# Optimization experiments

Measured on AMD Instinct MI355X. Metric: run time of the kernel, lower is better.

The kernel has to match this reference:

```python
import jax, jax.numpy as jnp
import numpy as np

B, T, D = 4, 2048, 512
H, P = 8, 16
DH = D // H
C = 512
HF = WF = 64
RADIUS = 0.08


def setup_inputs() -> dict:
    key = jax.random.key(0)
    ks = jax.random.split(key, 8)
    s = 0.02
    return {
        "q": jax.random.normal(ks[0], (B, T, D), jnp.float32),
        "fmap": jax.random.normal(ks[1], (B, C, HF, WF), jnp.float32),
        "ref_xy": jax.random.uniform(ks[2], (B, T, 2), jnp.float32),
        # params ((in,out) layout; equals torch Linear with W.T)
        "Wv": jax.random.normal(ks[3], (C, D), jnp.float32) * s,      # 1x1 conv, no bias
        "W_off": jax.random.normal(ks[4], (D, H * P * 2), jnp.float32) * s,
        "b_off": jnp.zeros((H * P * 2,), jnp.float32),
        "W_w": jax.random.normal(ks[5], (D, H * P), jnp.float32) * s,
        "b_w": jnp.zeros((H * P,), jnp.float32),
        "W_out": jax.random.normal(ks[6], (D, D), jnp.float32) * s,
        "b_out": jnp.zeros((D,), jnp.float32),
    }


def _deform_attn(q, fmap, ref_xy, Wv, W_off, b_off, W_w, b_w, W_out, b_out):
    Bq, Tq, Dm = q.shape
    _, Cc, Hf, Wf = fmap.shape
    dh = Dm // H
    # value projection (1x1 conv) then split heads: (B,H,dh,Hf,Wf)
    v = jnp.einsum("bchw,cd->bdhw", fmap, Wv).reshape(Bq, H, dh, Hf, Wf)
    # flatten spatial for gather: (B,H,Hf*Wf,dh)
    vflat = v.transpose(0, 1, 3, 4, 2).reshape(Bq, H, Hf * Wf, dh)

    off = (q @ W_off + b_off).reshape(Bq, Tq, H, P, 2)
    attn = jax.nn.softmax((q @ W_w + b_w).reshape(Bq, Tq, H, P), axis=-1)

    samp = ref_xy[:, :, None, None, :] + RADIUS * off   # (B,T,H,P,2) in ~[0,1]
    g = samp * 2.0 - 1.0                                 # grid coords in [-1,1]
    # align_corners=True mapping to pixel coords
    ix = (g[..., 0] + 1.0) * 0.5 * (Wf - 1)              # (B,T,H,P)
    iy = (g[..., 1] + 1.0) * 0.5 * (Hf - 1)
    ix0 = jnp.floor(ix)
    iy0 = jnp.floor(iy)
    fx = ix - ix0
    fy = iy - iy0
    ix0i = ix0.astype(jnp.int32)
    iy0i = iy0.astype(jnp.int32)

    def corner(xi, yi, wgt):
        # wgt: bilinear weight * attention weight, (B,T,H,P)
        valid = (xi >= 0) & (xi < Wf) & (yi >= 0) & (yi < Hf)  # zeros padding
        xi_c = jnp.clip(xi, 0, Wf - 1)
        yi_c = jnp.clip(yi, 0, Hf - 1)
        idx = (yi_c * Wf + xi_c).transpose(0, 2, 1, 3).reshape(Bq, H, Tq * P)
        gat = jnp.take_along_axis(vflat, idx[..., None], axis=2)  # (B,H,T*P,dh)
        wm = (wgt * valid).transpose(0, 2, 1, 3).reshape(Bq, H, Tq * P)
        return gat * wm[..., None]

    # fold softmax weights into bilinear corner weights, then sum over points
    feat = (
        corner(ix0i,     iy0i,     (1 - fx) * (1 - fy) * attn)
        + corner(ix0i + 1, iy0i,     fx * (1 - fy) * attn)
        + corner(ix0i,     iy0i + 1, (1 - fx) * fy * attn)
        + corner(ix0i + 1, iy0i + 1, fx * fy * attn)
    )  # (B,H,T*P,dh)
    ctx = feat.reshape(Bq, H, Tq, P, dh).sum(axis=3)     # (B,H,T,dh)
    ctx = ctx.transpose(0, 2, 1, 3).reshape(Bq, Tq, Dm)  # concat heads
    return ctx @ W_out + b_out


def reference(q, fmap, ref_xy, Wv, W_off, b_off, W_w, b_w, W_out, b_out):
    return _deform_attn(q, fmap, ref_xy, Wv, W_off, b_off, W_w, b_w, W_out, b_out)
```

## Files before the change

### kernel.cpp

```cpp
#include <hip/hip_runtime.h>
#include <hip/hip_bf16.h>
#include <math.h>

constexpr int Bsz = 4, T = 2048, Hh = 8;
constexpr int HFi = 64, WFi = 64;
constexpr float RADIUS = 0.08f;

typedef __bf16 bf16x8 __attribute__((ext_vector_type(8)));
typedef float f32x4 __attribute__((ext_vector_type(4)));
typedef unsigned short u16x8 __attribute__((ext_vector_type(8)));

typedef const __attribute__((address_space(1))) void* gcptr;
typedef __attribute__((address_space(3))) void* lptr;

#define GLOAD_LDS16(g, l) \
  __builtin_amdgcn_global_load_lds((gcptr)(const void*)(g), (lptr)(void*)(l), 16, 0, 0)

union BU { __hip_bfloat16 b; unsigned short u; };

__global__ __launch_bounds__(256) void prep_kernel(
    const float* __restrict__ q, __hip_bfloat16* __restrict__ qsplit,
    const float* __restrict__ W_off, const float* __restrict__ W_w,
    const float* __restrict__ b_off, const float* __restrict__ b_w,
    __hip_bfloat16* __restrict__ Wcat, float* __restrict__ bias_cat,
    const float* __restrict__ Wv, __hip_bfloat16* __restrict__ WvT,
    const float* __restrict__ W_out, __hip_bfloat16* __restrict__ WoutT,
    const float* __restrict__ fmap, __hip_bfloat16* __restrict__ fmapT) {
  __shared__ float tile[64][65];
  const int blk = blockIdx.x;
  const int tid = threadIdx.x;
  if (blk < 4096) {
    const int idx = blk * 256 + tid;
    const int m = idx >> 7, kq = (idx & 127) * 4;
    float4 v = *(const float4*)&q[(size_t)m * 512 + kq];
    union { __hip_bfloat16 b[4]; ushort4 u; } hi, lo;
    float f[4] = {v.x, v.y, v.z, v.w};
#pragma unroll
    for (int i = 0; i < 4; ++i) {
      hi.b[i] = __float2bfloat16(f[i]);
      lo.b[i] = __float2bfloat16(f[i] - __bfloat162float(hi.b[i]));
    }
    *(ushort4*)&qsplit[(size_t)m * 1024 + kq] = hi.u;
    *(ushort4*)&qsplit[(size_t)m * 1024 + 512 + kq] = lo.u;
    return;
  }
  if (blk < 6400) {
    const int idx = (blk - 4096) * 256 + tid;
    const int n = idx / 1536, kp = idx % 1536;
    const int k = kp & 511;
    const float w = (n < 256) ? W_off[(size_t)k * 256 + n]
                              : W_w[(size_t)k * 128 + (n - 256)];
    const __hip_bfloat16 h = __float2bfloat16(w);
    const __hip_bfloat16 o =
        (kp < 1024) ? h : __float2bfloat16(w - __bfloat162float(h));
    Wcat[(size_t)n * 1536 + kp] = o;
    if (idx < 384) bias_cat[idx] = (idx < 256) ? b_off[idx] : b_w[idx - 256];
    return;
  }
  const float* src;
  __hip_bfloat16* dst;
  int ldin, ldout, r0, c0;
  if (blk < 6528) {
    const int t2 = blk - 6400;
    src = (t2 < 64) ? Wv : W_out;
    dst = (t2 < 64) ? WvT : WoutT;
    ldin = 512; ldout = 512;
    const int tl = t2 & 63;
    r0 = (tl >> 3) * 64; c0 = (tl & 7) * 64;
  } else {
    const int t3 = blk - 6528;
    const int b = t3 >> 9;
    const int tl = t3 & 511;
    r0 = (tl >> 6) * 64;
    c0 = (tl & 63) * 64;
    src = fmap + (size_t)b * 512 * 4096;
    dst = fmapT + (size_t)b * 4096 * 512;
    ldin = 4096; ldout = 512;
  }
  {
    const int tr = tid >> 2;
    const int tc = (tid & 3) * 16;
    const float* s = &src[(size_t)(r0 + tr) * ldin + c0 + tc];
#pragma unroll
    for (int j4 = 0; j4 < 4; ++j4) {
      float4 v = *(const float4*)&s[j4 * 4];
      tile[tr][tc + j4 * 4 + 0] = v.x;
      tile[tr][tc + j4 * 4 + 1] = v.y;
      tile[tr][tc + j4 * 4 + 2] = v.z;
      tile[tr][tc + j4 * 4 + 3] = v.w;
    }
    __syncthreads();
    const int oc = tid >> 2;
    const int rb = (tid & 3) * 16;
    u16x8 o0, o1;
#pragma unroll
    for (int j = 0; j < 8; ++j) {
      BU a, bz;
      a.b = __float2bfloat16(tile[rb + j][oc]);
      bz.b = __float2bfloat16(tile[rb + 8 + j][oc]);
      o0[j] = a.u;
      o1[j] = bz.u;
    }
    __hip_bfloat16* d = &dst[(size_t)(c0 + oc) * ldout + r0 + rb];
    *(u16x8*)d = o0;
    *(u16x8*)(d + 8) = o1;
  }
}

__global__ __launch_bounds__(256) void fused_gemm(
    const __hip_bfloat16* __restrict__ qsplit,
    const __hip_bfloat16* __restrict__ Wcat,
    const float* __restrict__ bias_cat, float* __restrict__ projbuf,
    const __hip_bfloat16* __restrict__ fmapT,
    const __hip_bfloat16* __restrict__ WvT, __hip_bfloat16* __restrict__ vflat) {
  __shared__ unsigned short lds[2 * 128 * 64];
  unsigned short* As = lds;
  unsigned short* Bs = lds + 128 * 64;
  const int blk = blockIdx.x;
  const int tid = threadIdx.x;
  const int lane = tid & 63;
  const int wave = tid >> 6;
  const int l15 = lane & 15, quad = lane >> 4;
  const int srow = lane >> 3;
  const int scol = (((lane & 7) ^ srow) * 8);
  const int fxor = (l15 & 7) * 8;

  if (blk < 384) {
    const int m0 = (blk & 63) * 128;
    const int n0 = (blk >> 6) * 64;
    const int wm = (wave & 1) * 64, wn = (wave >> 1) * 32;
    f32x4 acc[4][2] = {};
    for (int k0 = 0; k0 < 1536; k0 += 64) {
      const int ka = (k0 >= 1024) ? k0 - 1024 : k0;
#pragma unroll
      for (int i = 0; i < 4; ++i) {
        const int j = wave * 4 + i;
        const int r = j * 8 + srow;
        GLOAD_LDS16(qsplit + (size_t)(m0 + r) * 1024 + ka + scol, As + j * 512);
      }
#pragma unroll
      for (int i = 0; i < 2; ++i) {
        const int j = wave * 2 + i;
        const int r = j * 8 + srow;
        GLOAD_LDS16(Wcat + (size_t)(n0 + r) * 1536 + k0 + scol, Bs + j * 512);
      }
      __syncthreads();
#pragma unroll
      for (int ks = 0; ks < 2; ++ks) {
        bf16x8 af[4], bfr[2];
#pragma unroll
        for (int i = 0; i < 4; ++i)
          af[i] = *(const bf16x8*)&As[(wm + i * 16 + l15) * 64 + ((ks * 32 + quad * 8) ^ fxor)];
#pragma unroll
        for (int j = 0; j < 2; ++j)
          bfr[j] = *(const bf16x8*)&Bs[(wn + j * 16 + l15) * 64 + ((ks * 32 + quad * 8) ^ fxor)];
#pragma unroll
        for (int i = 0; i < 4; ++i)
#pragma unroll
          for (int j = 0; j < 2; ++j)
            acc[i][j] = __builtin_amdgcn_mfma_f32_16x16x32_bf16(af[i], bfr[j], acc[i][j], 0, 0, 0);
      }
      __syncthreads();
    }
#pragma unroll
    for (int i = 0; i < 4; ++i) {
      const int mbase = m0 + wm + i * 16 + quad * 4;
#pragma unroll
      for (int j = 0; j < 2; ++j) {
        const int n = n0 + wn + j * 16 + l15;
        const float bb = bias_cat[n];
#pragma unroll
        for (int r = 0; r < 4; ++r)
          projbuf[(size_t)(mbase + r) * 384 + n] = acc[i][j][r] + bb;
      }
    }
  } else {
    const int vb = blk - 384;
    const int b = vb >> 7, rr = vb & 127;
    const int m0 = (rr >> 2) * 128;
    const int n0 = (rr & 3) * 128;
    const __hip_bfloat16* A = fmapT + (size_t)b * 4096 * 512;
    __hip_bfloat16* vout = vflat + (size_t)b * 8 * 4096 * 64;
    const int wm = (wave & 1) * 64, wn = (wave >> 1) * 64;
    f32x4 acc[4][4] = {};
    for (int k0 = 0; k0 < 512; k0 += 64) {
#pragma unroll
      for (int i = 0; i < 4; ++i) {
        const int j = wave * 4 + i;
        const int r = j * 8 + srow;
        GLOAD_LDS16(A + (size_t)(m0 + r) * 512 + k0 + scol, As + j * 512);
        GLOAD_LDS16(WvT + (size_t)(n0 + r) * 512 + k0 + scol, Bs + j * 512);
      }
      __syncthreads();
#pragma unroll
      for (int ks = 0; ks < 2; ++ks) {
        bf16x8 af[4], bfr[4];
#pragma unroll
        for (int i = 0; i < 4; ++i)
          af[i] = *(const bf16x8*)&As[(wm + i * 16 + l15) * 64 + ((ks * 32 + quad * 8) ^ fxor)];
#pragma unroll
        for (int j = 0; j < 4; ++j)
          bfr[j] = *(const bf16x8*)&Bs[(wn + j * 16 + l15) * 64 + ((ks * 32 + quad * 8) ^ fxor)];
#pragma unroll
        for (int i = 0; i < 4; ++i)
#pragma unroll
          for (int j = 0; j < 4; ++j)
            acc[i][j] = __builtin_amdgcn_mfma_f32_16x16x32_bf16(af[i], bfr[j], acc[i][j], 0, 0, 0);
      }
      __syncthreads();
    }
    unsigned short* Ct = lds;
#pragma unroll
    for (int i = 0; i < 4; ++i) {
#pragma unroll
      for (int j = 0; j < 4; ++j) {
        const int ngl = wn + j * 16 + l15;
#pragma unroll
        for (int r = 0; r < 4; ++r) {
          const int sl = wm + i * 16 + quad * 4 + r;
          BU u;
          u.b = __float2bfloat16(acc[i][j][r]);
          Ct[sl * 128 + (ngl ^ (((sl >> 2) & 3) * 16))] = u.u;
        }
      }
    }
    __syncthreads();
#pragma unroll
    for (int c = 0; c < 8; ++c) {
      const int sl = (tid >> 4) + c * 16;
      const int chunk = tid & 15;
      const int head = (n0 >> 6) + (chunk >> 3);
      const int dh = (chunk & 7) * 8;
      const int e = (chunk * 8) ^ (((sl >> 2) & 3) * 16);
      *(u16x8*)(vout + (size_t)head * (4096 * 64) + (size_t)(m0 + sl) * 64 + dh) =
          *(const u16x8*)&Ct[sl * 128 + e];
    }
  }
}

__global__ __launch_bounds__(256) void sample_kernel(
    const float* __restrict__ ref_xy, const float* __restrict__ projbuf,
    const unsigned int* __restrict__ vflat2, unsigned int* __restrict__ ctx2) {
  __shared__ float4 wsm[8][16];
  __shared__ int bsm[8][16];
  const int blk = blockIdx.x;
  const int bt = (blk & 7) * 1024 + (blk >> 3);
  const int b = bt >> 11;
  const int tid = threadIdx.x;
  const int wave = tid >> 6;
  const int lane = tid & 63;
  const int l31 = lane & 31;
  const bool hiHalf = lane >= 32;

  if (tid < 64) {
    const int h = tid >> 3, pi = tid & 7;
    const float ref_x = ref_xy[bt * 2 + 0];
    const float ref_y = ref_xy[bt * 2 + 1];
    const float* prow = projbuf + (size_t)bt * 384;
    const float* lg = prow + 256 + h * 16;
    float lv[16];
    float mx = -1e30f;
#pragma unroll
    for (int p = 0; p < 16; ++p) {
      lv[p] = lg[p];
      mx = fmaxf(mx, lv[p]);
    }
    float sum = 0.f;
#pragma unroll
    for (int p = 0; p < 16; ++p) {
      lv[p] = __expf(lv[p] - mx);
      sum += lv[p];
    }
    const float inv = 1.0f / sum;
    const float* of = prow + h * 32;
#pragma unroll
    for (int pq = 0; pq < 2; ++pq) {
      const int p = pi + pq * 8;
      const float aw = inv * lv[p];
      const float2 o2 = *(const float2*)&of[p * 2];
      const float ix = (ref_x + RADIUS * o2.x) * (float)(WFi - 1);
      const float iy = (ref_y + RADIUS * o2.y) * (float)(HFi - 1);
      const float ix0f = floorf(ix), iy0f = floorf(iy);
      const float fx = ix - ix0f, fy = iy - iy0f;
      const int ix0 = (int)ix0f, iy0 = (int)iy0f;

      float wx0 = 1.f - fx, wx1 = fx;
      float wy0 = 1.f - fy, wy1 = fy;
      if (ix0 == -1) { wx0 = fx; wx1 = 0.f; }
      if (ix0 == 63) { wx0 = 0.f; wx1 = 1.f - fx; }
      if (ix0 < -1 || ix0 > 63) { wx0 = 0.f; wx1 = 0.f; }
      if (iy0 == -1) { wy0 = fy; wy1 = 0.f; }
      if (iy0 == 63) { wy0 = 0.f; wy1 = 1.f - fy; }
      if (iy0 < -1 || iy0 > 63) { wy0 = 0.f; wy1 = 0.f; }
      const int xA = min(max(ix0, 0), WFi - 2);
      const int yA = min(max(iy0, 0), HFi - 2);

      wsm[h][p] = make_float4(wx0, wx1, wy0 * aw, wy1 * aw);
      bsm[h][p] = (yA * WFi + xA) * 32;
    }
  }
  __syncthreads();

  for (int h = wave; h < Hh; h += 4) {
    const float4* wq = &wsm[h][hiHalf ? 8 : 0];
    const int* bq = &bsm[h][hiHalf ? 8 : 0];
    const unsigned int* vb = vflat2 + (size_t)(b * 8 + h) * (4096 * 32) + l31;

    float acc0 = 0.f, acc1 = 0.f;
#pragma unroll
    for (int pp = 0; pp < 8; ++pp) {
      const float4 w4 = wq[pp];
      const unsigned int* r0 = vb + bq[pp];

      const unsigned int v00 = r0[0], v10 = r0[32];
      const unsigned int v01 = r0[2048], v11 = r0[2080];

      const float w00 = w4.x * w4.z, w10 = w4.y * w4.z;
      const float w01 = w4.x * w4.w, w11 = w4.y * w4.w;

      const float e00 = __uint_as_float(v00 << 16), o00 = __uint_as_float(v00 & 0xffff0000u);
      const float e10 = __uint_as_float(v10 << 16), o10 = __uint_as_float(v10 & 0xffff0000u);
      const float e01 = __uint_as_float(v01 << 16), o01 = __uint_as_float(v01 & 0xffff0000u);
      const float e11 = __uint_as_float(v11 << 16), o11 = __uint_as_float(v11 & 0xffff0000u);

      acc0 = fmaf(w00, e00, acc0);
      acc1 = fmaf(w00, o00, acc1);
      acc0 = fmaf(w10, e10, acc0);
      acc1 = fmaf(w10, o10, acc1);
      acc0 = fmaf(w01, e01, acc0);
      acc1 = fmaf(w01, o01, acc1);
      acc0 = fmaf(w11, e11, acc0);
      acc1 = fmaf(w11, o11, acc1);
    }

    acc0 += __shfl_xor(acc0, 32, 64);
    acc1 += __shfl_xor(acc1, 32, 64);
    if (!hiHalf) {
      BU c0, c1;
      c0.b = __float2bfloat16(acc0);
      c1.b = __float2bfloat16(acc1);
      ctx2[(size_t)bt * 256 + h * 32 + l31] = ((unsigned int)c1.u << 16) | c0.u;
    }
  }
}

__global__ __launch_bounds__(256) void outproj_kernel(
    const __hip_bfloat16* __restrict__ A, const __hip_bfloat16* __restrict__ Bm,
    const float* __restrict__ bias, float* __restrict__ C) {
  __shared__ unsigned short As[128 * 64];
  __shared__ unsigned short Bs[128 * 64];
  const int tid = threadIdx.x;
  const int lane = tid & 63;
  const int wave = tid >> 6;
  const int wm = (wave & 1) * 64, wn = (wave >> 1) * 64;
  const int l15 = lane & 15, quad = lane >> 4;
  const int m0 = blockIdx.x * 128, n0 = blockIdx.y * 128;
  const int srow = lane >> 3;
  const int scol = (((lane & 7) ^ srow) * 8);
  const int fxor = (l15 & 7) * 8;

  f32x4 acc[4][4] = {};

  for (int k0 = 0; k0 < 512; k0 += 64) {
#pragma unroll
    for (int i = 0; i < 4; ++i) {
      const int j = wave * 4 + i;
      const int r = j * 8 + srow;
      GLOAD_LDS16(A + (size_t)(m0 + r) * 512 + k0 + scol, As + j * 512);
      GLOAD_LDS16(Bm + (size_t)(n0 + r) * 512 + k0 + scol, Bs + j * 512);
    }
    __syncthreads();
#pragma unroll
    for (int ks = 0; ks < 2; ++ks) {
      bf16x8 af[4], bfr[4];
#pragma unroll
      for (int i = 0; i < 4; ++i)
        af[i] = *(const bf16x8*)&As[(wm + i * 16 + l15) * 64 + ((ks * 32 + quad * 8) ^ fxor)];
#pragma unroll
      for (int j = 0; j < 4; ++j)
        bfr[j] = *(const bf16x8*)&Bs[(wn + j * 16 + l15) * 64 + ((ks * 32 + quad * 8) ^ fxor)];
#pragma unroll
      for (int i = 0; i < 4; ++i)
#pragma unroll
        for (int j = 0; j < 4; ++j)
          acc[i][j] = __builtin_amdgcn_mfma_f32_16x16x32_bf16(af[i], bfr[j], acc[i][j], 0, 0, 0);
    }
    __syncthreads();
  }

#pragma unroll
  for (int i = 0; i < 4; ++i) {
    const int mbase = m0 + wm + i * 16 + quad * 4;
#pragma unroll
    for (int j = 0; j < 4; ++j) {
      const int n = n0 + wn + j * 16 + l15;
      const float bb = bias[n];
#pragma unroll
      for (int r = 0; r < 4; ++r)
        C[(size_t)(mbase + r) * 512 + n] = acc[i][j][r] + bb;
    }
  }
}

extern "C" void kernel_launch(void* const* d_in, const int* in_sizes, int n_in,
                              void* d_out, int out_size, void* d_ws, size_t ws_size,
                              hipStream_t stream) {
  const float* q      = (const float*)d_in[0];
  const float* fmap   = (const float*)d_in[1];
  const float* ref_xy = (const float*)d_in[2];
  const float* Wv     = (const float*)d_in[3];
  const float* W_off  = (const float*)d_in[4];
  const float* b_off  = (const float*)d_in[5];
  const float* W_w    = (const float*)d_in[6];
  const float* b_w    = (const float*)d_in[7];
  const float* W_out  = (const float*)d_in[8];
  const float* b_out  = (const float*)d_in[9];
  float* out = (float*)d_out;

  char* ws = (char*)d_ws;
  __hip_bfloat16* qsplit = (__hip_bfloat16*)ws; ws += (size_t)8192 * 1024 * 2;
  __hip_bfloat16* Wcat   = (__hip_bfloat16*)ws; ws += (size_t)384 * 1536 * 2;
  float* bias_cat        = (float*)ws;          ws += 384 * 4;
  float* projbuf         = (float*)ws;          ws += (size_t)8192 * 384 * 4;
  __hip_bfloat16* fmapT  = (__hip_bfloat16*)ws; ws += (size_t)4 * 4096 * 512 * 2;
  __hip_bfloat16* WvT    = (__hip_bfloat16*)ws; ws += (size_t)512 * 512 * 2;
  __hip_bfloat16* WoutT  = (__hip_bfloat16*)ws; ws += (size_t)512 * 512 * 2;
  __hip_bfloat16* vflat  = (__hip_bfloat16*)ws; ws += (size_t)4 * 8 * 4096 * 64 * 2;
  __hip_bfloat16* ctxb   = (__hip_bfloat16*)ws; ws += (size_t)8192 * 512 * 2;

  prep_kernel<<<dim3(8576), 256, 0, stream>>>(
      q, qsplit, W_off, W_w, b_off, b_w, Wcat, bias_cat, Wv, WvT, W_out, WoutT,
      fmap, fmapT);

  fused_gemm<<<dim3(896), 256, 0, stream>>>(
      qsplit, Wcat, bias_cat, projbuf, fmapT, WvT, vflat);

  sample_kernel<<<dim3(Bsz * T), 256, 0, stream>>>(
      ref_xy, projbuf, (const unsigned int*)vflat, (unsigned int*)ctxb);

  outproj_kernel<<<dim3(64, 4), 256, 0, stream>>>(ctxb, WoutT, b_out, out);
}
```

Measured before the change: 187.4 us.

## Restructure sampling kernel to one query per wave with 8-byte gathers

The sampling kernel now handles four queries per block, one per wave, instead of one query per block with a single 64-thread wave doing setup. The softmax over points is computed cooperatively with lane shuffles rather than serially per thread. Gathers use 8-byte uint2 loads (4 bf16 channels per lane), with 16 lanes covering a head row and four lane groups splitting the points, reduced by shuffles. This aims to use all threads in setup, cut block count and launch overhead, and widen memory accesses, at the cost of more shuffle reductions and more registers per lane.

New measurement: 192.0 us. 2.5% more time.

```diff
diff --git a/kernel.cpp b/kernel.cpp
--- a/kernel.cpp
+++ b/kernel.cpp
@@ -17,6 +17,13 @@
   __builtin_amdgcn_global_load_lds((gcptr)(const void*)(g), (lptr)(void*)(l), 16, 0, 0)
 
 union BU { __hip_bfloat16 b; unsigned short u; };
+
+__device__ __forceinline__ float bflo(unsigned int u) {
+  return __uint_as_float(u << 16);
+}
+__device__ __forceinline__ float bfhi(unsigned int u) {
+  return __uint_as_float(u & 0xffff0000u);
+}
 
 __global__ __launch_bounds__(256) void prep_kernel(
     const float* __restrict__ q, __hip_bfloat16* __restrict__ qsplit,
@@ -240,43 +247,38 @@
 
 __global__ __launch_bounds__(256) void sample_kernel(
     const float* __restrict__ ref_xy, const float* __restrict__ projbuf,
-    const unsigned int* __restrict__ vflat2, unsigned int* __restrict__ ctx2) {
-  __shared__ float4 wsm[8][16];
-  __shared__ int bsm[8][16];
+    const uint2* __restrict__ vflat2, uint2* __restrict__ ctx2) {
+  __shared__ float4 wsm[4][8][16];
+  __shared__ int bsm[4][8][16];
   const int blk = blockIdx.x;
-  const int bt = (blk & 7) * 1024 + (blk >> 3);
-  const int b = bt >> 11;
   const int tid = threadIdx.x;
   const int wave = tid >> 6;
   const int lane = tid & 63;
-  const int l31 = lane & 31;
-  const bool hiHalf = lane >= 32;
-
-  if (tid < 64) {
-    const int h = tid >> 3, pi = tid & 7;
+  const int bt = (blk & 7) * 1024 + (blk >> 3) * 4 + wave;
+  const int b = bt >> 11;
+
+  {
+    const int h = lane >> 3, pi = lane & 7;
     const float ref_x = ref_xy[bt * 2 + 0];
     const float ref_y = ref_xy[bt * 2 + 1];
     const float* prow = projbuf + (size_t)bt * 384;
     const float* lg = prow + 256 + h * 16;
-    float lv[16];
-    float mx = -1e30f;
-#pragma unroll
-    for (int p = 0; p < 16; ++p) {
-      lv[p] = lg[p];
-      mx = fmaxf(mx, lv[p]);
-    }
-    float sum = 0.f;
-#pragma unroll
-    for (int p = 0; p < 16; ++p) {
-      lv[p] = __expf(lv[p] - mx);
-      sum += lv[p];
-    }
-    const float inv = 1.0f / sum;
+    const float l0 = lg[pi], l1 = lg[pi + 8];
+    float mx = fmaxf(l0, l1);
+    mx = fmaxf(mx, __shfl_xor(mx, 1, 64));
+    mx = fmaxf(mx, __shfl_xor(mx, 2, 64));
+    mx = fmaxf(mx, __shfl_xor(mx, 4, 64));
+    const float e0 = __expf(l0 - mx), e1 = __expf(l1 - mx);
+    float s = e0 + e1;
+    s += __shfl_xor(s, 1, 64);
+    s += __shfl_xor(s, 2, 64);
+    s += __shfl_xor(s, 4, 64);
+    const float inv = 1.0f / s;
     const float* of = prow + h * 32;
 #pragma unroll
-    for (int pq = 0; pq < 2; ++pq) {
-      const int p = pi + pq * 8;
-      const float aw = inv * lv[p];
+    for (int q = 0; q < 2; ++q) {
+      const int p = pi + q * 8;
+      const float aw = inv * (q ? e1 : e0);
       const float2 o2 = *(const float2*)&of[p * 2];
       const float ix = (ref_x + RADIUS * o2.x) * (float)(WFi - 1);
       const float iy = (ref_y + RADIUS * o2.y) * (float)(HFi - 1);
@@ -295,51 +297,62 @@
       const int xA = min(max(ix0, 0), WFi - 2);
       const int yA = min(max(iy0, 0), HFi - 2);
 
-      wsm[h][p] = make_float4(wx0, wx1, wy0 * aw, wy1 * aw);
-      bsm[h][p] = (yA * WFi + xA) * 32;
+      wsm[wave][h][p] = make_float4(wx0, wx1, wy0 * aw, wy1 * aw);
+      bsm[wave][h][p] = (yA * WFi + xA) * 16;
     }
   }
   __syncthreads();
 
-  for (int h = wave; h < Hh; h += 4) {
-    const float4* wq = &wsm[h][hiHalf ? 8 : 0];
-    const int* bq = &bsm[h][hiHalf ? 8 : 0];
-    const unsigned int* vb = vflat2 + (size_t)(b * 8 + h) * (4096 * 32) + l31;
-
-    float acc0 = 0.f, acc1 = 0.f;
-#pragma unroll
-    for (int pp = 0; pp < 8; ++pp) {
-      const float4 w4 = wq[pp];
-      const unsigned int* r0 = vb + bq[pp];
-
-      const unsigned int v00 = r0[0], v10 = r0[32];
-      const unsigned int v01 = r0[2048], v11 = r0[2080];
-
+  const int g = lane >> 4, sub = lane & 15;
+#pragma unroll
+  for (int h = 0; h < Hh; ++h) {
+    const uint2* vb = vflat2 + (size_t)(b * 8 + h) * (4096 * 16) + sub;
+    float a0 = 0.f, a1 = 0.f, a2 = 0.f, a3 = 0.f;
+#pragma unroll
+    for (int it = 0; it < 4; ++it) {
+      const int p = g * 4 + it;
+      const float4 w4 = wsm[wave][h][p];
+      const int base = bsm[wave][h][p];
+      const uint2 v00 = vb[base], v10 = vb[base + 16];
+      const uint2 v01 = vb[base + 1024], v11 = vb[base + 1040];
       const float w00 = w4.x * w4.z, w10 = w4.y * w4.z;
       const float w01 = w4.x * w4.w, w11 = w4.y * w4.w;
 
-      const float e00 = __uint_as_float(v00 << 16), o00 = __uint_as_float(v00 & 0xffff0000u);
-      const float e10 = __uint_as_float(v10 << 16), o10 = __uint_as_float(v10 & 0xffff0000u);
-      const float e01 = __uint_as_float(v01 << 16), o01 = __uint_as_float(v01 & 0xffff0000u);
-      const float e11 = __uint_as_float(v11 << 16), o11 = __uint_as_float(v11 & 0xffff0000u);
-
-      acc0 = fmaf(w00, e00, acc0);
-      acc1 = fmaf(w00, o00, acc1);
-      acc0 = fmaf(w10, e10, acc0);
-      acc1 = fmaf(w10, o10, acc1);
-      acc0 = fmaf(w01, e01, acc0);
-      acc1 = fmaf(w01, o01, acc1);
-      acc0 = fmaf(w11, e11, acc0);
-      acc1 = fmaf(w11, o11, acc1);
-    }
-
-    acc0 += __shfl_xor(acc0, 32, 64);
-    acc1 += __shfl_xor(acc1, 32, 64);
-    if (!hiHalf) {
-      BU c0, c1;
-      c0.b = __float2bfloat16(acc0);
-      c1.b = __float2bfloat16(acc1);
-      ctx2[(size_t)bt * 256 + h * 32 + l31] = ((unsigned int)c1.u << 16) | c0.u;
+      a0 = fmaf(w00, bflo(v00.x), a0);
+      a1 = fmaf(w00, bfhi(v00.x), a1);
+      a2 = fmaf(w00, bflo(v00.y), a2);
+      a3 = fmaf(w00, bfhi(v00.y), a3);
+      a0 = fmaf(w10, bflo(v10.x), a0);
+      a1 = fmaf(w10, bfhi(v10.x), a1);
+      a2 = fmaf(w10, bflo(v10.y), a2);
+      a3 = fmaf(w10, bfhi(v10.y), a3);
+      a0 = fmaf(w01, bflo(v01.x), a0);
+      a1 = fmaf(w01, bfhi(v01.x), a1);
+      a2 = fmaf(w01, bflo(v01.y), a2);
+      a3 = fmaf(w01, bfhi(v01.y), a3);
+      a0 = fmaf(w11, bflo(v11.x), a0);
+      a1 = fmaf(w11, bfhi(v11.x), a1);
+      a2 = fmaf(w11, bflo(v11.y), a2);
+      a3 = fmaf(w11, bfhi(v11.y), a3);
+    }
+    a0 += __shfl_xor(a0, 16, 64);
+    a0 += __shfl_xor(a0, 32, 64);
+    a1 += __shfl_xor(a1, 16, 64);
+    a1 += __shfl_xor(a1, 32, 64);
+    a2 += __shfl_xor(a2, 16, 64);
+    a2 += __shfl_xor(a2, 32, 64);
+    a3 += __shfl_xor(a3, 16, 64);
+    a3 += __shfl_xor(a3, 32, 64);
+    if (g == 0) {
+      BU c0, c1, c2, c3;
+      c0.b = __float2bfloat16(a0);
+      c1.b = __float2bfloat16(a1);
+      c2.b = __float2bfloat16(a2);
+      c3.b = __float2bfloat16(a3);
+      uint2 ov;
+      ov.x = ((unsigned int)c1.u << 16) | c0.u;
+      ov.y = ((unsigned int)c3.u << 16) | c2.u;
+      ctx2[(size_t)bt * 128 + h * 16 + sub] = ov;
     }
   }
 }
@@ -435,8 +448,8 @@
   fused_gemm<<<dim3(896), 256, 0, stream>>>(
       qsplit, Wcat, bias_cat, projbuf, fmapT, WvT, vflat);
 
-  sample_kernel<<<dim3(Bsz * T), 256, 0, stream>>>(
-      ref_xy, projbuf, (const unsigned int*)vflat, (unsigned int*)ctxb);
+  sample_kernel<<<dim3(2048), 256, 0, stream>>>(
+      ref_xy, projbuf, (const uint2*)vflat, (uint2*)ctxb);
 
   outproj_kernel<<<dim3(64, 4), 256, 0, stream>>>(ctxb, WoutT, b_out, out);
 }
```
